# Kernel tuning notes

Measured on AMD Instinct MI355X. Metric: run time of the kernel, lower is better.

## Reference

```python
import jax, jax.numpy as jnp
import numpy as np

# Dims chosen per init_kwargs / input_specs
B, CIN, H, W = 16, 384, 64, 64
HEADS, HD = 4, 24
D = HEADS * HD                 # 96, per-pixel feature dim after head split
NMOD = 2                       # PartitionalClustering (hard), FuzzyClustering (soft)
NSTREAM = 1 + 2 * NMOD         # p + (k,v) per clustering module = 5
AG = 8                         # agents_hw = (8,8) -> 64 agent tokens
CL = 2                         # clusters_hw = (2,2) -> 4 clusters per module
M_PER = CL * CL
M_ALL = NMOD * M_PER           # 8 total clusters (sim_alpha/sim_beta size)


def setup_inputs() -> dict:
    key = jax.random.key(0)
    ks = jax.random.split(key, 4)
    x = jax.random.normal(ks[0], (B, CIN, H, W), jnp.float32)
    # proj: 1x1 pointwise linear CIN -> NSTREAM*D
    W1 = jax.random.normal(ks[1], (CIN, NSTREAM * D), jnp.float32) * 0.02
    b1 = jnp.zeros((NSTREAM * D,), jnp.float32)
    # proj2: 1x1 pointwise linear D -> CIN
    W2 = jax.random.normal(ks[2], (D, CIN), jnp.float32) * 0.02
    b2 = jnp.zeros((CIN,), jnp.float32)
    sim_alpha = jnp.ones((M_ALL,), jnp.float32)
    sim_beta = jnp.zeros((M_ALL,), jnp.float32)
    return {"x": x, "W1": W1, "b1": b1, "W2": W2, "b2": b2,
            "sim_alpha": sim_alpha, "sim_beta": sim_beta}


def _pool(t, oh, ow):
    # exact adaptive avg pool when h%oh==0 and w%ow==0
    b, c, h, w = t.shape
    return t.reshape(b, c, oh, h // oh, ow, w // ow).mean(axis=(3, 5))


def _cluster_agg(k, kc, v, vc, hard):
    # k: (b,c,N)  kc: (b,m,c)  v: (b,N,c)  vc: (b,m,c)
    # similarity = negative squared euclidean distance (use_cosine=False)
    d2 = (kc ** 2).sum(-1)[..., None] + (k ** 2).sum(1)[:, None, :] \
         - 2.0 * jnp.einsum('bmc,bcn->bmn', kc, k)          # (b,m,N)
    sim = -d2
    if hard:   # PartitionalClustering: hard one-hot assignment over clusters
        w = jax.nn.one_hot(jnp.argmax(sim, axis=1), sim.shape[1], axis=1, dtype=k.dtype)
    else:      # FuzzyClustering: soft assignment over clusters
        w = jax.nn.softmax(sim, axis=1)
    agg = vc + jnp.einsum('bmn,bnc->bmc', w, v)
    return agg / (1.0 + w.sum(-1, keepdims=True))            # cluster-bias normalization


def _cosine(a, p):
    # a: (b,M,c), p: (b,c,N) -> cosine similarity (b,M,N)
    an = a / (jnp.linalg.norm(a, axis=-1, keepdims=True) + 1e-6)
    pn = p / (jnp.linalg.norm(p, axis=1, keepdims=True) + 1e-6)
    return jnp.einsum('bmc,bcn->bmn', an, pn)


def reference(x, W1, b1, W2, b2, sim_alpha, sim_beta):
    # proj (1x1): (B,CIN,H,W) -> (B, NSTREAM*D, H, W)
    y = jnp.einsum('bchw,cd->bdhw', x, W1) + b1[None, :, None, None]
    b = B * HEADS
    y = y.reshape(B, NSTREAM, D, H, W).transpose(1, 0, 2, 3, 4)
    y = y.reshape(NSTREAM, b, HD, H, W)
    p = y[0]                                   # (b, HD, H, W)
    r = y[1:].reshape(NMOD, 2, b, HD, H, W)    # (module, k/v, b, HD, H, W)

    aggs = []
    for i in range(NMOD):
        k, v = r[i, 0], r[i, 1]
        kc = _pool(k, CL, CL).reshape(b, HD, M_PER).transpose(0, 2, 1)  # (b,m,c)
        vc = _pool(v, CL, CL).reshape(b, HD, M_PER).transpose(0, 2, 1)
        ka = _pool(k, AG, AG).reshape(b, HD, AG * AG)                   # (b,c,N)
        va = _pool(v, AG, AG).reshape(b, HD, AG * AG).transpose(0, 2, 1)
        aggs.append(_cluster_agg(ka, kc, va, vc, hard=(i == 0)))
    agg = jnp.concatenate(aggs, axis=1)        # (b, M_ALL, HD)

    pa = _pool(p, AG, AG).reshape(b, HD, AG * AG)                       # (b,c,N)
    sim = sim_alpha[None, :, None] * _cosine(agg, pa) + sim_beta[None, :, None]
    assign = jax.nn.softmax(sim, axis=1)        # over clusters
    out = jnp.einsum('bmc,bmn->bcn', agg, assign).reshape(b, HD, AG, AG)
    out = jax.image.resize(out, (b, HD, H, W), method='bilinear')
    out = out.reshape(B, D, H, W)
    # proj2 (1x1): D -> CIN
    return jnp.einsum('bchw,co->bohw', out, W2) + b2[None, :, None, None]
```

## Files before the change

### kernel.cpp

```cpp
#include <hip/hip_runtime.h>
#include <math.h>

#define NB     16
#define NCIN   384
#define NHD    24
#define NDIM   96
#define NSTR   5
#define NDT    480

__global__ void __launch_bounds__(256) k_pool(const float* __restrict__ x,
                                              float* __restrict__ x8) {
    int plane = blockIdx.x * 4 + (threadIdx.x >> 6);
    int lane  = threadIdx.x & 63;
    int py = lane >> 3, px = lane & 7;
    const float* base = x + (size_t)plane * 4096 + py * 8 * 64 + px * 8;
    float acc = 0.f;
#pragma unroll
    for (int rr = 0; rr < 8; ++rr) {
        float4 a = *reinterpret_cast<const float4*>(base + rr * 64);
        float4 b = *reinterpret_cast<const float4*>(base + rr * 64 + 4);
        acc += a.x + a.y + a.z + a.w + b.x + b.y + b.z + b.w;
    }
    x8[plane * 64 + lane] = acc * (1.f / 64.f);
}

#define KC 64
__global__ void __launch_bounds__(256) k_proj(const float* __restrict__ x8,
                                              const float* __restrict__ W1,
                                              const float* __restrict__ b1,
                                              float* __restrict__ y8) {
    __shared__ float AL[KC][32];
    __shared__ float BL[KC][64];
    const int b    = blockIdx.y >> 1;
    const int pix0 = (blockIdx.y & 1) * 32;
    const int d0   = blockIdx.x * 64;
    const int tid  = threadIdx.x;
    const int pxg  = (tid & 15) * 2;
    const int dg   = (tid >> 4) * 4;
    float acc[2][4] = {};
    for (int c0 = 0; c0 < 384; c0 += KC) {
        __syncthreads();
#pragma unroll
        for (int i = 0; i < 2; ++i) {
            int f = tid + i * 256;
            int c = f >> 3, pg = f & 7;
            *reinterpret_cast<float4*>(&AL[c][pg * 4]) =
                *reinterpret_cast<const float4*>(&x8[(b * 384 + c0 + c) * 64 + pix0 + pg * 4]);
        }
#pragma unroll
        for (int i = 0; i < 4; ++i) {
            int f = tid + i * 256;
            int c = f >> 4, jg = f & 15;
            int d = d0 + jg * 4;
            float4 v = make_float4(0.f, 0.f, 0.f, 0.f);
            if (d < NDT) v = *reinterpret_cast<const float4*>(&W1[(c0 + c) * NDT + d]);
            *reinterpret_cast<float4*>(&BL[c][jg * 4]) = v;
        }
        __syncthreads();
#pragma unroll 8
        for (int c = 0; c < KC; ++c) {
            float2 a = *reinterpret_cast<const float2*>(&AL[c][pxg]);
            float4 w = *reinterpret_cast<const float4*>(&BL[c][dg]);
            acc[0][0] += a.x * w.x; acc[0][1] += a.x * w.y;
            acc[0][2] += a.x * w.z; acc[0][3] += a.x * w.w;
            acc[1][0] += a.y * w.x; acc[1][1] += a.y * w.y;
            acc[1][2] += a.y * w.z; acc[1][3] += a.y * w.w;
        }
    }
    if (d0 + dg < NDT) {
        float4 bv = *reinterpret_cast<const float4*>(&b1[d0 + dg]);
#pragma unroll
        for (int p = 0; p < 2; ++p) {
            int pix = pix0 + pxg + p;
            float4 v = make_float4(acc[p][0] + bv.x, acc[p][1] + bv.y,
                                   acc[p][2] + bv.z, acc[p][3] + bv.w);
            *reinterpret_cast<float4*>(&y8[(size_t)(b * 64 + pix) * NDT + d0 + dg]) = v;
        }
    }
}

__global__ void __launch_bounds__(256) k_cluster(const float* __restrict__ y8,
                                                 const float* __restrict__ salpha,
                                                 const float* __restrict__ sbeta,
                                                 float* __restrict__ out8) {
    __shared__ float sl[5][64][25];
    __shared__ float y2s[5][4][24];
    __shared__ float wb[2][64][5];
    __shared__ float aggL[8][25];
    __shared__ float anL[8][24];
    __shared__ float normL[8];

    const int bp = blockIdx.x;
    const int Bi = bp >> 2, h = bp & 3;
    const int tid = threadIdx.x;
    const int lane = tid & 63, wid = tid >> 6;

    for (int idx = tid; idx < 5 * 64 * 24; idx += 256) {
        int c = idx % 24;
        int pix = (idx / 24) & 63;
        int s = idx / (24 * 64);
        sl[s][pix][c] = y8[(size_t)(Bi * 64 + pix) * NDT + s * NDIM + h * NHD + c];
    }
    __syncthreads();
    for (int idx = tid; idx < 5 * 4 * 24; idx += 256) {
        int c = idx % 24;
        int m = (idx / 24) & 3;
        int s = idx / 96;
        int my = m >> 1, mx = m & 1;
        float acc = 0.f;
        for (int ry = 0; ry < 4; ++ry)
            for (int rx = 0; rx < 4; ++rx)
                acc += sl[s][(my * 4 + ry) * 8 + mx * 4 + rx][c];
        y2s[s][m][c] = acc * (1.f / 16.f);
    }
    __syncthreads();
    if (wid < 2) {
        const int i = wid, ks = 1 + 2 * i;
        float ka[24];
        float sumk2 = 0.f;
#pragma unroll
        for (int c = 0; c < 24; ++c) { ka[c] = sl[ks][lane][c]; sumk2 += ka[c] * ka[c]; }
        float sim[4];
#pragma unroll
        for (int m = 0; m < 4; ++m) {
            float kc2 = 0.f, dt = 0.f;
#pragma unroll
            for (int c = 0; c < 24; ++c) {
                float kv = y2s[ks][m][c];
                kc2 += kv * kv; dt += kv * ka[c];
            }
            sim[m] = 2.f * dt - kc2 - sumk2;
        }
        float w[4];
        if (i == 0) {
            int am = 0; float bv = sim[0];
#pragma unroll
            for (int m = 1; m < 4; ++m) if (sim[m] > bv) { bv = sim[m]; am = m; }
#pragma unroll
            for (int m = 0; m < 4; ++m) w[m] = (m == am) ? 1.f : 0.f;
        } else {
            float mx = fmaxf(fmaxf(sim[0], sim[1]), fmaxf(sim[2], sim[3]));
            float sum = 0.f;
#pragma unroll
            for (int m = 0; m < 4; ++m) { w[m] = expf(sim[m] - mx); sum += w[m]; }
            float inv = 1.f / sum;
#pragma unroll
            for (int m = 0; m < 4; ++m) w[m] *= inv;
        }
#pragma unroll
        for (int m = 0; m < 4; ++m) wb[i][lane][m] = w[m];
    }
    __syncthreads();
    if (tid < 200) {
        int i = tid / 100, rem = tid % 100;
        int m = rem / 25, c = rem % 25;
        int vs = 2 + 2 * i;
        float s = 0.f;
        for (int n = 0; n < 64; ++n) {
            float wv = wb[i][n][m];
            s += (c < 24) ? wv * sl[vs][n][c] : wv;
        }
        aggL[i * 4 + m][c] = s;
    }
    __syncthreads();
    if (tid < 192) {
        int mm = tid / 24, c = tid % 24;
        int i = mm >> 2, m = mm & 3;
        aggL[mm][c] = (y2s[2 + 2 * i][m][c] + aggL[mm][c]) / (1.f + aggL[mm][24]);
    }
    __syncthreads();
    if (tid < 8) {
        float s = 0.f;
        for (int c = 0; c < 24; ++c) s += aggL[tid][c] * aggL[tid][c];
        normL[tid] = sqrtf(s) + 1e-6f;
    }
    __syncthreads();
    if (tid < 192) {
        int mm = tid / 24, c = tid % 24;
        anL[mm][c] = aggL[mm][c] / normL[mm];
    }
    __syncthreads();
    {
        const int n = lane;
        float pa[24]; float p2 = 0.f;
#pragma unroll
        for (int c = 0; c < 24; ++c) { pa[c] = sl[0][n][c]; p2 += pa[c] * pa[c]; }
        float pinv = 1.f / (sqrtf(p2) + 1e-6f);
        float s2[8];
#pragma unroll
        for (int mm = 0; mm < 8; ++mm) {
            float dt = 0.f;
#pragma unroll
            for (int c = 0; c < 24; ++c) dt += anL[mm][c] * pa[c];
            s2[mm] = salpha[mm] * (dt * pinv) + sbeta[mm];
        }
        float mx = s2[0];
#pragma unroll
        for (int mm = 1; mm < 8; ++mm) mx = fmaxf(mx, s2[mm]);
        float sum = 0.f;
#pragma unroll
        for (int mm = 0; mm < 8; ++mm) { s2[mm] = expf(s2[mm] - mx); sum += s2[mm]; }
        float inv = 1.f / sum;
        const int c0 = wid * 6;
#pragma unroll
        for (int cc = 0; cc < 6; ++cc) {
            int c = c0 + cc;
            float v = 0.f;
#pragma unroll
            for (int mm = 0; mm < 8; ++mm) v += aggL[mm][c] * (s2[mm] * inv);
            out8[(size_t)(Bi * NDIM + h * NHD + c) * 64 + n] = v;
        }
    }
}

__global__ void __launch_bounds__(256) k_proj2up(const float* __restrict__ out8,
                                                 const float* __restrict__ W2,
                                                 const float* __restrict__ b2,
                                                 float* __restrict__ out) {
    __shared__ float AL[96][64];
    __shared__ float WL[96][16];
    __shared__ float ZT[16][65];
    const int Bi = blockIdx.y;
    const int o0 = blockIdx.x * 16;
    const int tid = threadIdx.x;

#pragma unroll
    for (int i = 0; i < 6; ++i) {
        int f = tid + i * 256;
        int d = f >> 4, ng = f & 15;
        *reinterpret_cast<float4*>(&AL[d][ng * 4]) =
            *reinterpret_cast<const float4*>(&out8[(size_t)(Bi * NDIM + d) * 64 + ng * 4]);
    }
#pragma unroll
    for (int i = 0; i < 6; ++i) {
        int f = tid + i * 256;
        int d = f >> 4, o = f & 15;
        WL[d][o] = W2[d * NCIN + o0 + o];
    }
    __syncthreads();
    {
        const int n = tid & 63, og = tid >> 6;
        float acc0 = 0.f, acc1 = 0.f, acc2 = 0.f, acc3 = 0.f;
#pragma unroll 8
        for (int d = 0; d < 96; ++d) {
            float a = AL[d][n];
            float4 w = *reinterpret_cast<const float4*>(&WL[d][og * 4]);
            acc0 += a * w.x; acc1 += a * w.y; acc2 += a * w.z; acc3 += a * w.w;
        }
        __syncthreads();
        ZT[og * 4 + 0][n] = acc0;
        ZT[og * 4 + 1][n] = acc1;
        ZT[og * 4 + 2][n] = acc2;
        ZT[og * 4 + 3][n] = acc3;
    }
    __syncthreads();
    const int ol = tid >> 4, xq = tid & 15;
    const float bias = b2[o0 + ol];

    float uxb = 0.125f * (float)(xq * 4) - 0.4375f;
    float uxbc = fminf(fmaxf(uxb, 0.f), 7.f);
    const int ixb = (int)uxbc;
    float wa[4], wbx[4], wc[4];
#pragma unroll
    for (int j = 0; j < 4; ++j) {
        float ux  = 0.125f * (float)(xq * 4 + j) - 0.4375f;
        float uxc = fminf(fmaxf(ux, 0.f), 7.f);
        int ix0 = (int)uxc;
        int ix1 = ix0 + 1 > 7 ? 7 : ix0 + 1;
        float fx = uxc - (float)ix0;
        int k0 = ix0 - ixb, k1 = ix1 - ixb;
        wa[j]  = ((k0 == 0) ? (1.f - fx) : 0.f) + ((k1 == 0) ? fx : 0.f);
        wbx[j] = ((k0 == 1) ? (1.f - fx) : 0.f) + ((k1 == 1) ? fx : 0.f);
        wc[j]  = ((k1 == 2) ? fx : 0.f);
    }
    float zc0[8], zc1[8], zc2[8];
    {
        const int i1 = ixb + 1 > 7 ? 7 : ixb + 1;
        const int i2 = ixb + 2 > 7 ? 7 : ixb + 2;
#pragma unroll
        for (int iy = 0; iy < 8; ++iy) {
            zc0[iy] = ZT[ol][iy * 8 + ixb];
            zc1[iy] = ZT[ol][iy * 8 + i1];
            zc2[iy] = ZT[ol][iy * 8 + i2];
        }
    }
    float* obase = out + (size_t)(Bi * NCIN + o0 + ol) * 4096 + xq * 4;
#pragma unroll
    for (int y = 0; y < 64; ++y) {
        const float u  = 0.125f * (float)y - 0.4375f;
        const float uc = fminf(fmaxf(u, 0.f), 7.f);
        const int iy0 = (int)uc;
        const int iy1 = iy0 + 1 > 7 ? 7 : iy0 + 1;
        const float fy = uc - (float)iy0;
        const float r0 = zc0[iy0] + fy * (zc0[iy1] - zc0[iy0]);
        const float r1 = zc1[iy0] + fy * (zc1[iy1] - zc1[iy0]);
        const float r2 = zc2[iy0] + fy * (zc2[iy1] - zc2[iy0]);
        float4 v;
        v.x = bias + wa[0] * r0 + wbx[0] * r1 + wc[0] * r2;
        v.y = bias + wa[1] * r0 + wbx[1] * r1 + wc[1] * r2;
        v.z = bias + wa[2] * r0 + wbx[2] * r1 + wc[2] * r2;
        v.w = bias + wa[3] * r0 + wbx[3] * r1 + wc[3] * r2;
        *reinterpret_cast<float4*>(obase + y * 64) = v;
    }
}

extern "C" void kernel_launch(void* const* d_in, const int* in_sizes, int n_in,
                              void* d_out, int out_size, void* d_ws, size_t ws_size,
                              hipStream_t stream) {
    const float* x  = (const float*)d_in[0];
    const float* W1 = (const float*)d_in[1];
    const float* b1 = (const float*)d_in[2];
    const float* W2 = (const float*)d_in[3];
    const float* b2 = (const float*)d_in[4];
    const float* sa = (const float*)d_in[5];
    const float* sb = (const float*)d_in[6];
    float* out = (float*)d_out;

    float* x8 = (float*)d_ws;
    float* y8 = x8 + 16 * 384 * 64;
    float* o8 = y8 + 1024 * 480;

    k_pool<<<dim3(16 * 384 / 4), dim3(256), 0, stream>>>(x, x8);
    k_proj<<<dim3(8, 32), dim3(256), 0, stream>>>(x8, W1, b1, y8);
    k_cluster<<<dim3(64), dim3(256), 0, stream>>>(y8, sa, sb, o8);
    k_proj2up<<<dim3(24, 16), dim3(256), 0, stream>>>(o8, W2, b2, out);
}
```

Measured before the change: 67.34 us.

## Add nontemporal loads/stores, double-buffer projection GEMM, retile output projection

Input pooling now reads x with nontemporal loads, and the final upsampled output is written with nontemporal stores, so the large streaming traffic does not pollute the cache. The pointwise projection GEMM gains register-staged double buffering of its shared tiles, overlapping the next chunk's global loads with the current FMAs and dropping one barrier per iteration. The output projection is retiled from 16 to 12 channels per block, giving more blocks, but a quarter of the threads sit idle in the upsample phase. The cluster kernel also gets extra unroll pragmas.

```diff
diff --git a/kernel.cpp b/kernel.cpp
--- a/kernel.cpp
+++ b/kernel.cpp
@@ -8,17 +8,20 @@
 #define NSTR   5
 #define NDT    480
 
+typedef float nfloat4 __attribute__((ext_vector_type(4)));
+
 __global__ void __launch_bounds__(256) k_pool(const float* __restrict__ x,
                                               float* __restrict__ x8) {
     int plane = blockIdx.x * 4 + (threadIdx.x >> 6);
     int lane  = threadIdx.x & 63;
     int py = lane >> 3, px = lane & 7;
-    const float* base = x + (size_t)plane * 4096 + py * 8 * 64 + px * 8;
+    const nfloat4* base = reinterpret_cast<const nfloat4*>(x) +
+                          (size_t)plane * 1024 + py * 128 + px * 2;
     float acc = 0.f;
 #pragma unroll
     for (int rr = 0; rr < 8; ++rr) {
-        float4 a = *reinterpret_cast<const float4*>(base + rr * 64);
-        float4 b = *reinterpret_cast<const float4*>(base + rr * 64 + 4);
+        nfloat4 a = __builtin_nontemporal_load(base + rr * 16);
+        nfloat4 b = __builtin_nontemporal_load(base + rr * 16 + 1);
         acc += a.x + a.y + a.z + a.w + b.x + b.y + b.z + b.w;
     }
     x8[plane * 64 + lane] = acc * (1.f / 64.f);
@@ -29,43 +32,54 @@
                                               const float* __restrict__ W1,
                                               const float* __restrict__ b1,
                                               float* __restrict__ y8) {
-    __shared__ float AL[KC][32];
-    __shared__ float BL[KC][64];
+    __shared__ float AL[2][KC][32];
+    __shared__ float BL[2][KC][64];
     const int b    = blockIdx.y >> 1;
     const int pix0 = (blockIdx.y & 1) * 32;
     const int d0   = blockIdx.x * 64;
     const int tid  = threadIdx.x;
     const int pxg  = (tid & 15) * 2;
     const int dg   = (tid >> 4) * 4;
+
+    const int ca0 = (tid) >> 3,        pga0 = (tid) & 7;
+    const int ca1 = (tid + 256) >> 3,  pga1 = (tid + 256) & 7;
+    int cb[4], jgb[4];
+#pragma unroll
+    for (int i = 0; i < 4; ++i) { int f = tid + i * 256; cb[i] = f >> 4; jgb[i] = f & 15; }
+
+    float4 ra[2], rb[4];
+    auto load_chunk = [&](int c0) {
+        ra[0] = *reinterpret_cast<const float4*>(&x8[(b * 384 + c0 + ca0) * 64 + pix0 + pga0 * 4]);
+        ra[1] = *reinterpret_cast<const float4*>(&x8[(b * 384 + c0 + ca1) * 64 + pix0 + pga1 * 4]);
+#pragma unroll
+        for (int i = 0; i < 4; ++i) {
+            int d = d0 + jgb[i] * 4;
+            rb[i] = (d < NDT) ? *reinterpret_cast<const float4*>(&W1[(c0 + cb[i]) * NDT + d])
+                              : make_float4(0.f, 0.f, 0.f, 0.f);
+        }
+    };
+
     float acc[2][4] = {};
-    for (int c0 = 0; c0 < 384; c0 += KC) {
+    load_chunk(0);
+    int cur = 0;
+    for (int k = 0; k < 6; ++k) {
+        *reinterpret_cast<float4*>(&AL[cur][ca0][pga0 * 4]) = ra[0];
+        *reinterpret_cast<float4*>(&AL[cur][ca1][pga1 * 4]) = ra[1];
+#pragma unroll
+        for (int i = 0; i < 4; ++i)
+            *reinterpret_cast<float4*>(&BL[cur][cb[i]][jgb[i] * 4]) = rb[i];
         __syncthreads();
-#pragma unroll
-        for (int i = 0; i < 2; ++i) {
-            int f = tid + i * 256;
-            int c = f >> 3, pg = f & 7;
-            *reinterpret_cast<float4*>(&AL[c][pg * 4]) =
-                *reinterpret_cast<const float4*>(&x8[(b * 384 + c0 + c) * 64 + pix0 + pg * 4]);
-        }
-#pragma unroll
-        for (int i = 0; i < 4; ++i) {
-            int f = tid + i * 256;
-            int c = f >> 4, jg = f & 15;
-            int d = d0 + jg * 4;
-            float4 v = make_float4(0.f, 0.f, 0.f, 0.f);
-            if (d < NDT) v = *reinterpret_cast<const float4*>(&W1[(c0 + c) * NDT + d]);
-            *reinterpret_cast<float4*>(&BL[c][jg * 4]) = v;
-        }
-        __syncthreads();
+        if (k < 5) load_chunk((k + 1) * KC);
 #pragma unroll 8
         for (int c = 0; c < KC; ++c) {
-            float2 a = *reinterpret_cast<const float2*>(&AL[c][pxg]);
-            float4 w = *reinterpret_cast<const float4*>(&BL[c][dg]);
+            float2 a = *reinterpret_cast<const float2*>(&AL[cur][c][pxg]);
+            float4 w = *reinterpret_cast<const float4*>(&BL[cur][c][dg]);
             acc[0][0] += a.x * w.x; acc[0][1] += a.x * w.y;
             acc[0][2] += a.x * w.z; acc[0][3] += a.x * w.w;
             acc[1][0] += a.y * w.x; acc[1][1] += a.y * w.y;
             acc[1][2] += a.y * w.z; acc[1][3] += a.y * w.w;
         }
+        cur ^= 1;
     }
     if (d0 + dg < NDT) {
         float4 bv = *reinterpret_cast<const float4*>(&b1[d0 + dg]);
@@ -95,6 +109,7 @@
     const int tid = threadIdx.x;
     const int lane = tid & 63, wid = tid >> 6;
 
+#pragma unroll
     for (int idx = tid; idx < 5 * 64 * 24; idx += 256) {
         int c = idx % 24;
         int pix = (idx / 24) & 63;
@@ -102,13 +117,16 @@
         sl[s][pix][c] = y8[(size_t)(Bi * 64 + pix) * NDT + s * NDIM + h * NHD + c];
     }
     __syncthreads();
+#pragma unroll
     for (int idx = tid; idx < 5 * 4 * 24; idx += 256) {
         int c = idx % 24;
         int m = (idx / 24) & 3;
         int s = idx / 96;
         int my = m >> 1, mx = m & 1;
         float acc = 0.f;
+#pragma unroll
         for (int ry = 0; ry < 4; ++ry)
+#pragma unroll
             for (int rx = 0; rx < 4; ++rx)
                 acc += sl[s][(my * 4 + ry) * 8 + mx * 4 + rx][c];
         y2s[s][m][c] = acc * (1.f / 16.f);
@@ -156,6 +174,7 @@
         int m = rem / 25, c = rem % 25;
         int vs = 2 + 2 * i;
         float s = 0.f;
+#pragma unroll 8
         for (int n = 0; n < 64; ++n) {
             float wv = wb[i][n][m];
             s += (c < 24) ? wv * sl[vs][n][c] : wv;
@@ -171,6 +190,7 @@
     __syncthreads();
     if (tid < 8) {
         float s = 0.f;
+#pragma unroll
         for (int c = 0; c < 24; ++c) s += aggL[tid][c] * aggL[tid][c];
         normL[tid] = sqrtf(s) + 1e-6f;
     }
@@ -218,10 +238,10 @@
                                                  const float* __restrict__ b2,
                                                  float* __restrict__ out) {
     __shared__ float AL[96][64];
-    __shared__ float WL[96][16];
-    __shared__ float ZT[16][65];
+    __shared__ float WL[96][12];
+    __shared__ float ZT[12][65];
     const int Bi = blockIdx.y;
-    const int o0 = blockIdx.x * 16;
+    const int o0 = blockIdx.x * 12;
     const int tid = threadIdx.x;
 
 #pragma unroll
@@ -232,75 +252,75 @@
             *reinterpret_cast<const float4*>(&out8[(size_t)(Bi * NDIM + d) * 64 + ng * 4]);
     }
 #pragma unroll
-    for (int i = 0; i < 6; ++i) {
-        int f = tid + i * 256;
-        int d = f >> 4, o = f & 15;
+    for (int idx = tid; idx < 96 * 12; idx += 256) {
+        int d = idx / 12, o = idx - d * 12;
         WL[d][o] = W2[d * NCIN + o0 + o];
     }
     __syncthreads();
     {
         const int n = tid & 63, og = tid >> 6;
-        float acc0 = 0.f, acc1 = 0.f, acc2 = 0.f, acc3 = 0.f;
+        float a0 = 0.f, a1 = 0.f, a2 = 0.f;
 #pragma unroll 8
         for (int d = 0; d < 96; ++d) {
             float a = AL[d][n];
-            float4 w = *reinterpret_cast<const float4*>(&WL[d][og * 4]);
-            acc0 += a * w.x; acc1 += a * w.y; acc2 += a * w.z; acc3 += a * w.w;
-        }
-        __syncthreads();
-        ZT[og * 4 + 0][n] = acc0;
-        ZT[og * 4 + 1][n] = acc1;
-        ZT[og * 4 + 2][n] = acc2;
-        ZT[og * 4 + 3][n] = acc3;
-    }
-    __syncthreads();
-    const int ol = tid >> 4, xq = tid & 15;
-    const float bias = b2[o0 + ol];
-
-    float uxb = 0.125f * (float)(xq * 4) - 0.4375f;
-    float uxbc = fminf(fmaxf(uxb, 0.f), 7.f);
-    const int ixb = (int)uxbc;
-    float wa[4], wbx[4], wc[4];
-#pragma unroll
-    for (int j = 0; j < 4; ++j) {
-        float ux  = 0.125f * (float)(xq * 4 + j) - 0.4375f;
-        float uxc = fminf(fmaxf(ux, 0.f), 7.f);
-        int ix0 = (int)uxc;
-        int ix1 = ix0 + 1 > 7 ? 7 : ix0 + 1;
-        float fx = uxc - (float)ix0;
-        int k0 = ix0 - ixb, k1 = ix1 - ixb;
-        wa[j]  = ((k0 == 0) ? (1.f - fx) : 0.f) + ((k1 == 0) ? fx : 0.f);
-        wbx[j] = ((k0 == 1) ? (1.f - fx) : 0.f) + ((k1 == 1) ? fx : 0.f);
-        wc[j]  = ((k1 == 2) ? fx : 0.f);
-    }
-    float zc0[8], zc1[8], zc2[8];
-    {
-        const int i1 = ixb + 1 > 7 ? 7 : ixb + 1;
-        const int i2 = ixb + 2 > 7 ? 7 : ixb + 2;
-#pragma unroll
-        for (int iy = 0; iy < 8; ++iy) {
-            zc0[iy] = ZT[ol][iy * 8 + ixb];
-            zc1[iy] = ZT[ol][iy * 8 + i1];
-            zc2[iy] = ZT[ol][iy * 8 + i2];
-        }
-    }
-    float* obase = out + (size_t)(Bi * NCIN + o0 + ol) * 4096 + xq * 4;
-#pragma unroll
-    for (int y = 0; y < 64; ++y) {
-        const float u  = 0.125f * (float)y - 0.4375f;
-        const float uc = fminf(fmaxf(u, 0.f), 7.f);
-        const int iy0 = (int)uc;
-        const int iy1 = iy0 + 1 > 7 ? 7 : iy0 + 1;
-        const float fy = uc - (float)iy0;
-        const float r0 = zc0[iy0] + fy * (zc0[iy1] - zc0[iy0]);
-        const float r1 = zc1[iy0] + fy * (zc1[iy1] - zc1[iy0]);
-        const float r2 = zc2[iy0] + fy * (zc2[iy1] - zc2[iy0]);
-        float4 v;
-        v.x = bias + wa[0] * r0 + wbx[0] * r1 + wc[0] * r2;
-        v.y = bias + wa[1] * r0 + wbx[1] * r1 + wc[1] * r2;
-        v.z = bias + wa[2] * r0 + wbx[2] * r1 + wc[2] * r2;
-        v.w = bias + wa[3] * r0 + wbx[3] * r1 + wc[3] * r2;
-        *reinterpret_cast<float4*>(obase + y * 64) = v;
+            a0 += a * WL[d][og * 3 + 0];
+            a1 += a * WL[d][og * 3 + 1];
+            a2 += a * WL[d][og * 3 + 2];
+        }
+        ZT[og * 3 + 0][n] = a0;
+        ZT[og * 3 + 1][n] = a1;
+        ZT[og * 3 + 2][n] = a2;
+    }
+    __syncthreads();
+    if (tid < 192) {
+        const int ol = tid >> 4, xq = tid & 15;
+        const float bias = b2[o0 + ol];
+
+        float uxb = 0.125f * (float)(xq * 4) - 0.4375f;
+        float uxbc = fminf(fmaxf(uxb, 0.f), 7.f);
+        const int ixb = (int)uxbc;
+        float wa[4], wbx[4], wc[4];
+#pragma unroll
+        for (int j = 0; j < 4; ++j) {
+            float ux  = 0.125f * (float)(xq * 4 + j) - 0.4375f;
+            float uxc = fminf(fmaxf(ux, 0.f), 7.f);
+            int ix0 = (int)uxc;
+            int ix1 = ix0 + 1 > 7 ? 7 : ix0 + 1;
+            float fx = uxc - (float)ix0;
+            int k0 = ix0 - ixb, k1 = ix1 - ixb;
+            wa[j]  = ((k0 == 0) ? (1.f - fx) : 0.f) + ((k1 == 0) ? fx : 0.f);
+            wbx[j] = ((k0 == 1) ? (1.f - fx) : 0.f) + ((k1 == 1) ? fx : 0.f);
+            wc[j]  = ((k1 == 2) ? fx : 0.f);
+        }
+        float zc0[8], zc1[8], zc2[8];
+        {
+            const int i1 = ixb + 1 > 7 ? 7 : ixb + 1;
+            const int i2 = ixb + 2 > 7 ? 7 : ixb + 2;
+#pragma unroll
+            for (int iy = 0; iy < 8; ++iy) {
+                zc0[iy] = ZT[ol][iy * 8 + ixb];
+                zc1[iy] = ZT[ol][iy * 8 + i1];
+                zc2[iy] = ZT[ol][iy * 8 + i2];
+            }
+        }
+        float* obase = out + (size_t)(Bi * NCIN + o0 + ol) * 4096 + xq * 4;
+#pragma unroll
+        for (int y = 0; y < 64; ++y) {
+            const float u  = 0.125f * (float)y - 0.4375f;
+            const float uc = fminf(fmaxf(u, 0.f), 7.f);
+            const int iy0 = (int)uc;
+            const int iy1 = iy0 + 1 > 7 ? 7 : iy0 + 1;
+            const float fy = uc - (float)iy0;
+            const float r0 = zc0[iy0] + fy * (zc0[iy1] - zc0[iy0]);
+            const float r1 = zc1[iy0] + fy * (zc1[iy1] - zc1[iy0]);
+            const float r2 = zc2[iy0] + fy * (zc2[iy1] - zc2[iy0]);
+            nfloat4 v;
+            v.x = bias + wa[0] * r0 + wbx[0] * r1 + wc[0] * r2;
+            v.y = bias + wa[1] * r0 + wbx[1] * r1 + wc[1] * r2;
+            v.z = bias + wa[2] * r0 + wbx[2] * r1 + wc[2] * r2;
+            v.w = bias + wa[3] * r0 + wbx[3] * r1 + wc[3] * r2;
+            __builtin_nontemporal_store(v, reinterpret_cast<nfloat4*>(obase + y * 64));
+        }
     }
 }
 
@@ -323,5 +343,5 @@
     k_pool<<<dim3(16 * 384 / 4), dim3(256), 0, stream>>>(x, x8);
     k_proj<<<dim3(8, 32), dim3(256), 0, stream>>>(x8, W1, b1, y8);
     k_cluster<<<dim3(64), dim3(256), 0, stream>>>(y8, sa, sb, o8);
-    k_proj2up<<<dim3(24, 16), dim3(256), 0, stream>>>(o8, W2, b2, out);
-}
+    k_proj2up<<<dim3(32, 16), dim3(256), 0, stream>>>(o8, W2, b2, out);
+}
```

New measurement: 72.79 us. 8.1% more time.

## Coalesce pooling loads, vectorize cluster/W2 loads, widen proj2up output tile

Applied to the files above, without the earlier changes.

k_pool now uses one block per plane, with fully coalesced float4 row reads reduced through shared memory, instead of strided per-thread 8x8 window reads. k_cluster loads y8 with float4 and unrolls several small loops. k_proj2up handles 24 output channels per block instead of 16, giving fewer blocks and less repeated loading of the activation tile, and uses vectorized W2 loads. The 24-channel tile needs two passes for the upsample stores, leaving half the threads idle in the second pass, and the larger grid for k_pool adds more block scheduling.

```diff
diff --git a/kernel.cpp b/kernel.cpp
--- a/kernel.cpp
+++ b/kernel.cpp
@@ -10,18 +10,27 @@
 
 __global__ void __launch_bounds__(256) k_pool(const float* __restrict__ x,
                                               float* __restrict__ x8) {
-    int plane = blockIdx.x * 4 + (threadIdx.x >> 6);
-    int lane  = threadIdx.x & 63;
-    int py = lane >> 3, px = lane & 7;
-    const float* base = x + (size_t)plane * 4096 + py * 8 * 64 + px * 8;
-    float acc = 0.f;
-#pragma unroll
-    for (int rr = 0; rr < 8; ++rr) {
-        float4 a = *reinterpret_cast<const float4*>(base + rr * 64);
-        float4 b = *reinterpret_cast<const float4*>(base + rr * 64 + 4);
-        acc += a.x + a.y + a.z + a.w + b.x + b.y + b.z + b.w;
-    }
-    x8[plane * 64 + lane] = acc * (1.f / 64.f);
+    __shared__ float part[64][17];
+    const int plane = blockIdx.x;
+    const int t = threadIdx.x;
+    const float4* xp = reinterpret_cast<const float4*>(x + (size_t)plane * 4096);
+    const int chunk = t & 15;
+    const int rloc  = t >> 4;
+#pragma unroll
+    for (int rr = 0; rr < 4; ++rr) {
+        int row = rr * 16 + rloc;
+        float4 v = xp[rr * 256 + t];
+        part[row][chunk] = v.x + v.y + v.z + v.w;
+    }
+    __syncthreads();
+    if (t < 64) {
+        int py = t >> 3, px = t & 7;
+        float s = 0.f;
+#pragma unroll
+        for (int r = 0; r < 8; ++r)
+            s += part[py * 8 + r][px * 2] + part[py * 8 + r][px * 2 + 1];
+        x8[(size_t)plane * 64 + t] = s * (1.f / 64.f);
+    }
 }
 
 #define KC 64
@@ -95,11 +104,17 @@
     const int tid = threadIdx.x;
     const int lane = tid & 63, wid = tid >> 6;
 
-    for (int idx = tid; idx < 5 * 64 * 24; idx += 256) {
-        int c = idx % 24;
-        int pix = (idx / 24) & 63;
-        int s = idx / (24 * 64);
-        sl[s][pix][c] = y8[(size_t)(Bi * 64 + pix) * NDT + s * NDIM + h * NHD + c];
+    for (int idx = tid; idx < 5 * 64 * 6; idx += 256) {
+        int q = idx % 6;
+        int row = idx / 6;
+        int pix = row & 63, s = row >> 6;
+        float4 v = *reinterpret_cast<const float4*>(
+            &y8[(size_t)(Bi * 64 + pix) * NDT + s * NDIM + h * NHD + q * 4]);
+        int c = q * 4;
+        sl[s][pix][c]     = v.x;
+        sl[s][pix][c + 1] = v.y;
+        sl[s][pix][c + 2] = v.z;
+        sl[s][pix][c + 3] = v.w;
     }
     __syncthreads();
     for (int idx = tid; idx < 5 * 4 * 24; idx += 256) {
@@ -108,7 +123,9 @@
         int s = idx / 96;
         int my = m >> 1, mx = m & 1;
         float acc = 0.f;
+#pragma unroll
         for (int ry = 0; ry < 4; ++ry)
+#pragma unroll
             for (int rx = 0; rx < 4; ++rx)
                 acc += sl[s][(my * 4 + ry) * 8 + mx * 4 + rx][c];
         y2s[s][m][c] = acc * (1.f / 16.f);
@@ -156,6 +173,7 @@
         int m = rem / 25, c = rem % 25;
         int vs = 2 + 2 * i;
         float s = 0.f;
+#pragma unroll 8
         for (int n = 0; n < 64; ++n) {
             float wv = wb[i][n][m];
             s += (c < 24) ? wv * sl[vs][n][c] : wv;
@@ -171,6 +189,7 @@
     __syncthreads();
     if (tid < 8) {
         float s = 0.f;
+#pragma unroll
         for (int c = 0; c < 24; ++c) s += aggL[tid][c] * aggL[tid][c];
         normL[tid] = sqrtf(s) + 1e-6f;
     }
@@ -218,10 +237,10 @@
                                                  const float* __restrict__ b2,
                                                  float* __restrict__ out) {
     __shared__ float AL[96][64];
-    __shared__ float WL[96][16];
-    __shared__ float ZT[16][65];
+    __shared__ float WL[96][24];
+    __shared__ float ZT[24][65];
     const int Bi = blockIdx.y;
-    const int o0 = blockIdx.x * 16;
+    const int o0 = blockIdx.x * 24;
     const int tid = threadIdx.x;
 
 #pragma unroll
@@ -231,76 +250,86 @@
         *reinterpret_cast<float4*>(&AL[d][ng * 4]) =
             *reinterpret_cast<const float4*>(&out8[(size_t)(Bi * NDIM + d) * 64 + ng * 4]);
     }
-#pragma unroll
-    for (int i = 0; i < 6; ++i) {
-        int f = tid + i * 256;
-        int d = f >> 4, o = f & 15;
-        WL[d][o] = W2[d * NCIN + o0 + o];
+    for (int idx = tid; idx < 96 * 6; idx += 256) {
+        int d = idx / 6, q = idx % 6;
+        *reinterpret_cast<float4*>(&WL[d][q * 4]) =
+            *reinterpret_cast<const float4*>(&W2[d * NCIN + o0 + q * 4]);
     }
     __syncthreads();
     {
         const int n = tid & 63, og = tid >> 6;
-        float acc0 = 0.f, acc1 = 0.f, acc2 = 0.f, acc3 = 0.f;
+        float a0 = 0.f, a1 = 0.f, a2 = 0.f, a3 = 0.f, a4 = 0.f, a5 = 0.f;
 #pragma unroll 8
         for (int d = 0; d < 96; ++d) {
             float a = AL[d][n];
-            float4 w = *reinterpret_cast<const float4*>(&WL[d][og * 4]);
-            acc0 += a * w.x; acc1 += a * w.y; acc2 += a * w.z; acc3 += a * w.w;
-        }
-        __syncthreads();
-        ZT[og * 4 + 0][n] = acc0;
-        ZT[og * 4 + 1][n] = acc1;
-        ZT[og * 4 + 2][n] = acc2;
-        ZT[og * 4 + 3][n] = acc3;
-    }
-    __syncthreads();
-    const int ol = tid >> 4, xq = tid & 15;
-    const float bias = b2[o0 + ol];
-
-    float uxb = 0.125f * (float)(xq * 4) - 0.4375f;
-    float uxbc = fminf(fmaxf(uxb, 0.f), 7.f);
-    const int ixb = (int)uxbc;
-    float wa[4], wbx[4], wc[4];
-#pragma unroll
-    for (int j = 0; j < 4; ++j) {
-        float ux  = 0.125f * (float)(xq * 4 + j) - 0.4375f;
-        float uxc = fminf(fmaxf(ux, 0.f), 7.f);
-        int ix0 = (int)uxc;
-        int ix1 = ix0 + 1 > 7 ? 7 : ix0 + 1;
-        float fx = uxc - (float)ix0;
-        int k0 = ix0 - ixb, k1 = ix1 - ixb;
-        wa[j]  = ((k0 == 0) ? (1.f - fx) : 0.f) + ((k1 == 0) ? fx : 0.f);
-        wbx[j] = ((k0 == 1) ? (1.f - fx) : 0.f) + ((k1 == 1) ? fx : 0.f);
-        wc[j]  = ((k1 == 2) ? fx : 0.f);
-    }
-    float zc0[8], zc1[8], zc2[8];
-    {
-        const int i1 = ixb + 1 > 7 ? 7 : ixb + 1;
-        const int i2 = ixb + 2 > 7 ? 7 : ixb + 2;
-#pragma unroll
-        for (int iy = 0; iy < 8; ++iy) {
-            zc0[iy] = ZT[ol][iy * 8 + ixb];
-            zc1[iy] = ZT[ol][iy * 8 + i1];
-            zc2[iy] = ZT[ol][iy * 8 + i2];
-        }
-    }
-    float* obase = out + (size_t)(Bi * NCIN + o0 + ol) * 4096 + xq * 4;
-#pragma unroll
-    for (int y = 0; y < 64; ++y) {
-        const float u  = 0.125f * (float)y - 0.4375f;
-        const float uc = fminf(fmaxf(u, 0.f), 7.f);
-        const int iy0 = (int)uc;
-        const int iy1 = iy0 + 1 > 7 ? 7 : iy0 + 1;
-        const float fy = uc - (float)iy0;
-        const float r0 = zc0[iy0] + fy * (zc0[iy1] - zc0[iy0]);
-        const float r1 = zc1[iy0] + fy * (zc1[iy1] - zc1[iy0]);
-        const float r2 = zc2[iy0] + fy * (zc2[iy1] - zc2[iy0]);
-        float4 v;
-        v.x = bias + wa[0] * r0 + wbx[0] * r1 + wc[0] * r2;
-        v.y = bias + wa[1] * r0 + wbx[1] * r1 + wc[1] * r2;
-        v.z = bias + wa[2] * r0 + wbx[2] * r1 + wc[2] * r2;
-        v.w = bias + wa[3] * r0 + wbx[3] * r1 + wc[3] * r2;
-        *reinterpret_cast<float4*>(obase + y * 64) = v;
+            float2 w01 = *reinterpret_cast<const float2*>(&WL[d][og * 6 + 0]);
+            float2 w23 = *reinterpret_cast<const float2*>(&WL[d][og * 6 + 2]);
+            float2 w45 = *reinterpret_cast<const float2*>(&WL[d][og * 6 + 4]);
+            a0 += a * w01.x; a1 += a * w01.y;
+            a2 += a * w23.x; a3 += a * w23.y;
+            a4 += a * w45.x; a5 += a * w45.y;
+        }
+        ZT[og * 6 + 0][n] = a0;
+        ZT[og * 6 + 1][n] = a1;
+        ZT[og * 6 + 2][n] = a2;
+        ZT[og * 6 + 3][n] = a3;
+        ZT[og * 6 + 4][n] = a4;
+        ZT[og * 6 + 5][n] = a5;
+    }
+    __syncthreads();
+#pragma unroll
+    for (int pass = 0; pass < 2; ++pass) {
+        int slot = pass * 256 + tid;
+        if (slot < 24 * 16) {
+            const int ol = slot >> 4, xq = slot & 15;
+            const float bias = b2[o0 + ol];
+
+            float uxb = 0.125f * (float)(xq * 4) - 0.4375f;
+            float uxbc = fminf(fmaxf(uxb, 0.f), 7.f);
+            const int ixb = (int)uxbc;
+            float wa[4], wbx[4], wc[4];
+#pragma unroll
+            for (int j = 0; j < 4; ++j) {
+                float ux  = 0.125f * (float)(xq * 4 + j) - 0.4375f;
+                float uxc = fminf(fmaxf(ux, 0.f), 7.f);
+                int ix0 = (int)uxc;
+                int ix1 = ix0 + 1 > 7 ? 7 : ix0 + 1;
+                float fx = uxc - (float)ix0;
+                int k0 = ix0 - ixb, k1 = ix1 - ixb;
+                wa[j]  = ((k0 == 0) ? (1.f - fx) : 0.f) + ((k1 == 0) ? fx : 0.f);
+                wbx[j] = ((k0 == 1) ? (1.f - fx) : 0.f) + ((k1 == 1) ? fx : 0.f);
+                wc[j]  = ((k1 == 2) ? fx : 0.f);
+            }
+            float zc0[8], zc1[8], zc2[8];
+            {
+                const int i1 = ixb + 1 > 7 ? 7 : ixb + 1;
+                const int i2 = ixb + 2 > 7 ? 7 : ixb + 2;
+#pragma unroll
+                for (int iy = 0; iy < 8; ++iy) {
+                    zc0[iy] = ZT[ol][iy * 8 + ixb];
+                    zc1[iy] = ZT[ol][iy * 8 + i1];
+                    zc2[iy] = ZT[ol][iy * 8 + i2];
+                }
+            }
+            float* obase = out + (size_t)(Bi * NCIN + o0 + ol) * 4096 + xq * 4;
+#pragma unroll
+            for (int y = 0; y < 64; ++y) {
+                const float u  = 0.125f * (float)y - 0.4375f;
+                const float uc = fminf(fmaxf(u, 0.f), 7.f);
+                const int iy0 = (int)uc;
+                const int iy1 = iy0 + 1 > 7 ? 7 : iy0 + 1;
+                const float fy = uc - (float)iy0;
+                const float r0 = zc0[iy0] + fy * (zc0[iy1] - zc0[iy0]);
+                const float r1 = zc1[iy0] + fy * (zc1[iy1] - zc1[iy0]);
+                const float r2 = zc2[iy0] + fy * (zc2[iy1] - zc2[iy0]);
+                float4 v;
+                v.x = bias + wa[0] * r0 + wbx[0] * r1 + wc[0] * r2;
+                v.y = bias + wa[1] * r0 + wbx[1] * r1 + wc[1] * r2;
+                v.z = bias + wa[2] * r0 + wbx[2] * r1 + wc[2] * r2;
+                v.w = bias + wa[3] * r0 + wbx[3] * r1 + wc[3] * r2;
+                *reinterpret_cast<float4*>(obase + y * 64) = v;
+            }
+        }
     }
 }
 
@@ -320,8 +349,8 @@
     float* y8 = x8 + 16 * 384 * 64;
     float* o8 = y8 + 1024 * 480;
 
-    k_pool<<<dim3(16 * 384 / 4), dim3(256), 0, stream>>>(x, x8);
+    k_pool<<<dim3(16 * 384), dim3(256), 0, stream>>>(x, x8);
     k_proj<<<dim3(8, 32), dim3(256), 0, stream>>>(x8, W1, b1, y8);
     k_cluster<<<dim3(64), dim3(256), 0, stream>>>(y8, sa, sb, o8);
-    k_proj2up<<<dim3(24, 16), dim3(256), 0, stream>>>(o8, W2, b2, out);
-}
+    k_proj2up<<<dim3(16, 16), dim3(256), 0, stream>>>(o8, W2, b2, out);
+}
```

After: 68.30 us. About the same (+1.4%).
